# Kernel optimization log

Hardware: AMD Instinct MI355X
Metric: run time of the kernel (lower is better)

## Reference

```python
import jax, jax.numpy as jnp
import numpy as np

B, H, T, D = 4, 8, 4096, 64
NC = 64      # num_clusters
WSZ = 128    # window_size (== context_window_size)
MEM = 1      # num_mem_kv
EPS = 1e-5   # scatter_mean eps


def setup_inputs() -> dict:
    key = jax.random.key(0)
    kq, kk, kv, km, kmk, kmv = jax.random.split(key, 6)
    return {
        "q": jax.random.normal(kq, (B, H, T, D), jnp.float32),
        "k": jax.random.normal(kk, (B, H, T, D), jnp.float32),
        "v": jax.random.normal(kv, (B, H, T, D), jnp.float32),
        "means": jax.random.normal(km, (H, NC, D), jnp.float32),
        "mem_key": jax.random.normal(kmk, (H, NC, MEM, D), jnp.float32),
        "mem_value": jax.random.normal(kmv, (H, NC, MEM, D), jnp.float32),
    }


def reference(q, k, v, means, mem_key, mem_value):
    b, h, t, d = q.shape
    kv_t = k.shape[2]
    nc = means.shape[1]
    wsz = min(WSZ, t)
    kv_wsz = min(WSZ, kv_t)

    # --- kmeans routing (eval mode: no update, world_size=1) ---
    x = jnp.concatenate([q, k], axis=2)                       # (b,h,t+kv_t,d)
    norm = jnp.linalg.norm(x, axis=-1, keepdims=True)
    xn = x / jnp.maximum(norm, 1e-12)                          # F.normalize
    dists = jnp.einsum('bhld,hcd->bhlc', xn, means)            # (b,h,L,nc)
    buckets = jnp.argmax(dists, axis=-1)                       # (b,h,L)
    routed = means[jnp.arange(h)[None, :, None], buckets]      # (b,h,L,d)
    aux_loss = jnp.mean((xn - routed) ** 2)                    # mse / world_size(=1)

    dists = jax.lax.stop_gradient(dists)                       # torch no_grad
    q_dists, k_dists = dists[:, :, :t], dists[:, :, t:]

    def top_idx(dd, w):
        # dd: (b,h,L,nc) -> per-cluster top-w token indices, (b,h,nc*w)
        _, idx = jax.lax.top_k(jnp.swapaxes(dd, -1, -2), w)    # (b,h,nc,w)
        return idx.reshape(idx.shape[0], idx.shape[1], -1)

    indices = top_idx(q_dists, wsz)                            # (b,h,nc*wsz)
    kv_indices = top_idx(k_dists, kv_wsz)

    gather = lambda arr, idx: jnp.take_along_axis(arr, idx[..., None], axis=2)
    qg = gather(q, indices).reshape(b, h, nc, wsz, d)
    kg = gather(k, kv_indices).reshape(b, h, nc, kv_wsz, d)
    vg = gather(v, kv_indices).reshape(b, h, nc, kv_wsz, d)

    m_k = jnp.broadcast_to(mem_key[None], (b,) + mem_key.shape)
    m_v = jnp.broadcast_to(mem_value[None], (b,) + mem_value.shape)
    kg = jnp.concatenate([m_k, kg], axis=3)                    # (b,h,nc,MEM+kv_wsz,d)
    vg = jnp.concatenate([m_v, vg], axis=3)

    dots = jnp.einsum('bhnid,bhnjd->bhnij', qg, kg) * (d ** -0.5)
    attn = jax.nn.softmax(dots, axis=-1)
    bo = jnp.einsum('bhnij,bhnjd->bhnid', attn, vg)            # (b,h,nc,wsz,d)
    so = bo.reshape(b, h, nc * wsz, d)

    # scatter_mean back to token positions
    bi = jnp.arange(b)[:, None, None]
    hi = jnp.arange(h)[None, :, None]
    numer = jnp.zeros((b, h, t, d), q.dtype).at[bi, hi, indices].add(so)
    denom = jnp.zeros((b, h, t, d), q.dtype).at[bi, hi, indices].add(jnp.ones_like(so))
    out = numer / (denom + EPS)
    return out, aux_loss
```

## Files before the change

kernel.cpp:

```cpp
#include <hip/hip_runtime.h>
#include <math.h>

#define BB 4
#define HH 8
#define TT 4096
#define DD 64
#define NCC 64
#define WSZW 128
#define TPK 160
#define MEMN 1
#define KVW (MEMN + WSZW)
constexpr float EPSF = 1e-5f;
constexpr float SCALE = 0.125f;

typedef __attribute__((ext_vector_type(8))) short bf16x8;
typedef __attribute__((ext_vector_type(4))) float f32x4;

static __device__ __forceinline__ unsigned int pk2(float a, float b) {
    unsigned int r;
    asm("v_cvt_pk_bf16_f32 %0, %1, %2" : "=v"(r) : "v"(a), "v"(b));
    return r;
}
static __device__ __forceinline__ bf16x8 pack8(float4 a, float4 b) {
    union { unsigned int u[4]; bf16x8 v; } r;
    r.u[0] = pk2(a.x, a.y); r.u[1] = pk2(a.z, a.w);
    r.u[2] = pk2(b.x, b.y); r.u[3] = pk2(b.z, b.w);
    return r.v;
}
static __device__ __forceinline__ unsigned mono(float f) {
    unsigned b = __float_as_uint(f);
    return b ^ ((unsigned)(((int)b) >> 31) | 0x80000000u);
}
static __device__ __forceinline__ unsigned long long mono64(double d) {
    unsigned long long b = (unsigned long long)__double_as_longlong(d);
    return b ^ (((long long)b < 0) ? ~0ULL : 0x8000000000000000ULL);
}
static __device__ __forceinline__ float bf2f(unsigned short u) {
    return __uint_as_float(((unsigned)u) << 16);
}

__global__ __launch_bounds__(256, 4) void dists_kernel(
    const float* __restrict__ q, const float* __restrict__ k,
    const float* __restrict__ means,
    float* __restrict__ distsQ, float* __restrict__ distsK,
    float* __restrict__ aux_part, double* __restrict__ invn)
{
    __shared__ __align__(16) unsigned short mhS[64 * 64];
    __shared__ __align__(16) unsigned short mlS[64 * 64];
    __shared__ __align__(16) unsigned short xhS[64 * 64];
    __shared__ __align__(16) unsigned short xlS[64 * 64];
    __shared__ float mqS[64];
    __shared__ float ssnS[64];
    __shared__ float wMaxS[64 * 5];
    __shared__ int   wIdxS[64 * 5];

    const int chunks = (2 * TT) / 64;
    int bid0 = blockIdx.x;
    int bid = (bid0 & 7) * 512 + (bid0 >> 3);
    int bh = bid / chunks;
    int chunk = bid % chunks;
    int h = bh % HH;
    bool isQ = chunk < (TT / 64);
    int tbase = (isQ ? chunk : chunk - 64) * 64;
    const float* src = (isQ ? q : k) + ((size_t)bh * TT + tbase) * DD;
    float* dst = isQ ? distsQ : distsK;
    double* invdst = invn + (isQ ? 0 : (size_t)BB * HH * TT) + (size_t)bh * TT + tbase;

    int tid = threadIdx.x;
    int row = tid >> 2, part = tid & 3;

    {
        const float* mp = means + ((size_t)h * NCC + row) * DD + part * 16;
        float f[16];
        float msq = 0.f;
        #pragma unroll
        for (int i = 0; i < 4; ++i) {
            float4 va = *(const float4*)(mp + i * 4);
            f[i*4] = va.x; f[i*4+1] = va.y; f[i*4+2] = va.z; f[i*4+3] = va.w;
            msq += va.x*va.x + va.y*va.y + va.z*va.z + va.w*va.w;
        }
        msq += __shfl_xor(msq, 1);
        msq += __shfl_xor(msq, 2);
        if (part == 0) mqS[row] = msq;
        #pragma unroll
        for (int cc = 0; cc < 2; ++cc) {
            unsigned hw[4], lw[4];
            #pragma unroll
            for (int j2 = 0; j2 < 4; ++j2) {
                float a = f[cc*8 + j2*2], b = f[cc*8 + j2*2 + 1];
                unsigned p = pk2(a, b);
                float ha = __uint_as_float(p << 16);
                float hb = __uint_as_float(p & 0xFFFF0000u);
                hw[j2] = p; lw[j2] = pk2(a - ha, b - hb);
            }
            int ch = part * 2 + cc;
            int phys = ch ^ (row & 7);
            *reinterpret_cast<uint4*>(&mhS[row * 64 + phys * 8]) = (uint4){hw[0],hw[1],hw[2],hw[3]};
            *reinterpret_cast<uint4*>(&mlS[row * 64 + phys * 8]) = (uint4){lw[0],lw[1],lw[2],lw[3]};
        }
    }
    {
        const float* xp = src + (size_t)row * DD + part * 16;
        float f[16];
        double ssd = 0.0;
        #pragma unroll
        for (int i = 0; i < 4; ++i) {
            float4 va = *(const float4*)(xp + i * 4);
            f[i*4] = va.x; f[i*4+1] = va.y; f[i*4+2] = va.z; f[i*4+3] = va.w;
            ssd += (double)va.x*va.x + (double)va.y*va.y
                 + (double)va.z*va.z + (double)va.w*va.w;
        }
        ssd += __shfl_xor(ssd, 1);
        ssd += __shfl_xor(ssd, 2);
        double invd = 1.0 / fmax(sqrt(ssd), 1e-12);
        if (part == 0) {
            invdst[row] = invd;
            ssnS[row] = (float)(ssd * invd * invd);
        }
        float inv = (float)invd;
        #pragma unroll
        for (int i = 0; i < 16; ++i) f[i] *= inv;
        #pragma unroll
        for (int cc = 0; cc < 2; ++cc) {
            unsigned hw[4], lw[4];
            #pragma unroll
            for (int j2 = 0; j2 < 4; ++j2) {
                float a = f[cc*8 + j2*2], b = f[cc*8 + j2*2 + 1];
                unsigned p = pk2(a, b);
                float ha = __uint_as_float(p << 16);
                float hb = __uint_as_float(p & 0xFFFF0000u);
                hw[j2] = p; lw[j2] = pk2(a - ha, b - hb);
            }
            int ch = part * 2 + cc;
            int phys = ch ^ (row & 7);
            *reinterpret_cast<uint4*>(&xhS[row * 64 + phys * 8]) = (uint4){hw[0],hw[1],hw[2],hw[3]};
            *reinterpret_cast<uint4*>(&xlS[row * 64 + phys * 8]) = (uint4){lw[0],lw[1],lw[2],lw[3]};
        }
    }
    __syncthreads();

    int l = tid & 63, w = tid >> 6;
    int lr = l & 15, lg = l >> 4;

    bf16x8 mhF[2], mlF[2];
    #pragma unroll
    for (int ks = 0; ks < 2; ++ks) {
        int r2 = w * 16 + lr;
        int phys = (ks * 4 + lg) ^ (r2 & 7);
        mhF[ks] = *reinterpret_cast<const bf16x8*>(&mhS[r2 * 64 + phys * 8]);
        mlF[ks] = *reinterpret_cast<const bf16x8*>(&mlS[r2 * 64 + phys * 8]);
    }

    f32x4 accT[4];
    size_t rowb = (size_t)(bh * NCC) * TT;
    #pragma unroll
    for (int tt = 0; tt < 4; ++tt) {
        bf16x8 xhF[2], xlF[2];
        #pragma unroll
        for (int ks = 0; ks < 2; ++ks) {
            int r2 = tt * 16 + lr;
            int phys = (ks * 4 + lg) ^ (r2 & 7);
            xhF[ks] = *reinterpret_cast<const bf16x8*>(&xhS[r2 * 64 + phys * 8]);
            xlF[ks] = *reinterpret_cast<const bf16x8*>(&xlS[r2 * 64 + phys * 8]);
        }
        f32x4 a = (f32x4){0.f, 0.f, 0.f, 0.f};
        #pragma unroll
        for (int ks = 0; ks < 2; ++ks)
            a = __builtin_amdgcn_mfma_f32_16x16x32_bf16(mhF[ks], xhF[ks], a, 0, 0, 0);
        #pragma unroll
        for (int ks = 0; ks < 2; ++ks)
            a = __builtin_amdgcn_mfma_f32_16x16x32_bf16(mhF[ks], xlF[ks], a, 0, 0, 0);
        #pragma unroll
        for (int ks = 0; ks < 2; ++ks)
            a = __builtin_amdgcn_mfma_f32_16x16x32_bf16(mlF[ks], xhF[ks], a, 0, 0, 0);
        accT[tt] = a;
        #pragma unroll
        for (int r2 = 0; r2 < 4; ++r2) {
            int c = w * 16 + lg * 4 + r2;
            dst[rowb + (size_t)c * TT + tbase + tt * 16 + lr] = a[r2];
        }
    }

    #pragma unroll
    for (int tt = 0; tt < 4; ++tt) {
        float bv = accT[tt][0]; int bc = w * 16 + lg * 4;
        #pragma unroll
        for (int r2 = 1; r2 < 4; ++r2)
            if (accT[tt][r2] > bv) { bv = accT[tt][r2]; bc = w * 16 + lg * 4 + r2; }
        #pragma unroll
        for (int off = 16; off <= 32; off <<= 1) {
            float ov = __shfl_xor(bv, off);
            int   oc = __shfl_xor(bc, off);
            if (ov > bv || (ov == bv && oc < bc)) { bv = ov; bc = oc; }
        }
        if (lg == 0) {
            wMaxS[(tt * 16 + lr) * 5 + w] = bv;
            wIdxS[(tt * 16 + lr) * 5 + w] = bc;
        }
    }
    __syncthreads();

    if (tid < 64) {
        float bv = -1e30f; int bc = 0;
        #pragma unroll
        for (int w2 = 0; w2 < 4; ++w2) {
            float ov = wMaxS[tid * 5 + w2];
            int   oc = wIdxS[tid * 5 + w2];
            if (ov > bv || (ov == bv && oc < bc)) { bv = ov; bc = oc; }
        }
        float auxv = ssnS[tid] + mqS[bc] - 2.f * bv;
        #pragma unroll
        for (int off = 32; off; off >>= 1) auxv += __shfl_xor(auxv, off);
        if (tid == 0) aux_part[bid] = auxv;
    }
}

__global__ __launch_bounds__(256) void topk_kernel(
    const float* __restrict__ dists, int* __restrict__ idxOut)
{
    int row = blockIdx.x;
    const float* dv = dists + (size_t)row * TT;
    int t = threadIdx.x;
    int lane = t & 63, w = t >> 6;

    unsigned u[16];
    #pragma unroll
    for (int j0 = 0; j0 < 4; ++j0) {
        float4 f = *(const float4*)(dv + t * 16 + j0 * 4);
        u[j0*4+0] = mono(f.x); u[j0*4+1] = mono(f.y);
        u[j0*4+2] = mono(f.z); u[j0*4+3] = mono(f.w);
    }

    __shared__ int hist[4096];
    __shared__ int wtot[4];
    __shared__ int binSel, tgtS;
    __shared__ int nGtS, posS, eqPos;

    int target = TPK;
    unsigned prefix = 0;

    #pragma unroll
    for (int pass = 0; pass < 2; ++pass) {
        int4* hz = (int4*)&hist[t * 16];
        hz[0] = (int4){0,0,0,0}; hz[1] = (int4){0,0,0,0};
        hz[2] = (int4){0,0,0,0}; hz[3] = (int4){0,0,0,0};
        __syncthreads();
        if (pass == 0) {
            #pragma unroll
            for (int j = 0; j < 16; ++j) atomicAdd(&hist[u[j] >> 20], 1);
        } else {
            #pragma unroll
            for (int j = 0; j < 16; ++j)
                if ((u[j] >> 20) == (prefix >> 20))
                    atomicAdd(&hist[(u[j] >> 8) & 0xFFF], 1);
        }
        __syncthreads();
        int cnt[16], ls[16];
        {
            const int4* hp = (const int4*)&hist[t * 16];
            int4 c0 = hp[0], c1 = hp[1], c2 = hp[2], c3 = hp[3];
            cnt[0]=c0.x; cnt[1]=c0.y; cnt[2]=c0.z; cnt[3]=c0.w;
            cnt[4]=c1.x; cnt[5]=c1.y; cnt[6]=c1.z; cnt[7]=c1.w;
            cnt[8]=c2.x; cnt[9]=c2.y; cnt[10]=c2.z; cnt[11]=c2.w;
            cnt[12]=c3.x; cnt[13]=c3.y; cnt[14]=c3.z; cnt[15]=c3.w;
        }
        int run = 0;
        #pragma unroll
        for (int i = 15; i >= 0; --i) { run += cnt[i]; ls[i] = run; }
        int S = run;
        #pragma unroll
        for (int off = 1; off < 64; off <<= 1) {
            int o = __shfl_down(S, off);
            if (lane + off < 64) S += o;
        }
        if (lane == 0) wtot[w] = S;
        __syncthreads();
        int after = 0;
        for (int ww = w + 1; ww < 4; ++ww) after += wtot[ww];
        int St1 = S - run + after;
        #pragma unroll
        for (int i = 0; i < 16; ++i) {
            int sfxb = ls[i] + St1;
            if (sfxb >= target && sfxb - cnt[i] < target) {
                binSel = t * 16 + i; tgtS = target - (sfxb - cnt[i]);
            }
        }
        __syncthreads();
        prefix |= (pass == 0) ? ((unsigned)binSel << 20) : ((unsigned)binSel << 8);
        target = tgtS;
        __syncthreads();
    }

    hist[t] = 0;
    __syncthreads();
    #pragma unroll
    for (int j = 0; j < 16; ++j)
        if ((u[j] >> 8) == (prefix >> 8))
            atomicAdd(&hist[u[j] & 0xFF], 1);
    __syncthreads();
    {
        int cnt = hist[t];
        int S = cnt;
        #pragma unroll
        for (int off = 1; off < 64; off <<= 1) {
            int o = __shfl_down(S, off);
            if (lane + off < 64) S += o;
        }
        if (lane == 0) wtot[w] = S;
        __syncthreads();
        int after = 0;
        for (int ww = w + 1; ww < 4; ++ww) after += wtot[ww];
        int sfx = S + after;
        if (sfx >= target && sfx - cnt < target) { binSel = t; tgtS = target - (sfx - cnt); }
    }
    __syncthreads();
    unsigned pivot = prefix | (unsigned)binSel;

    if (t == 0) { nGtS = 0; posS = 0; eqPos = 0; }
    __syncthreads();
    int myg = 0;
    #pragma unroll
    for (int j = 0; j < 16; ++j) myg += (u[j] > pivot) ? 1 : 0;
    if (myg) atomicAdd(&nGtS, myg);
    __syncthreads();
    int n_gt = nGtS;
    int n_need = TPK - n_gt;
    int* out = idxOut + (size_t)row * TPK;
    #pragma unroll
    for (int j = 0; j < 16; ++j) {
        if (u[j] > pivot) {
            int p = atomicAdd(&posS, 1);
            out[p] = t * 16 + j;
        } else if (u[j] == pivot) {
            int p = atomicAdd(&eqPos, 1);
            if (p < n_need) out[n_gt + p] = t * 16 + j;
        }
    }
}

__global__ __launch_bounds__(640) void rescore_kernel(
    const float* __restrict__ q, const float* __restrict__ k,
    const float* __restrict__ means, const double* __restrict__ invn,
    const int* __restrict__ candQ, const int* __restrict__ candK,
    int* __restrict__ idxQ, int* __restrict__ idxK,
    int* __restrict__ counts)
{
    int bid = blockIdx.x;
    int rid = (bid & 7) * 512 + (bid >> 3);
    int side = rid >> 11;
    int row = rid & 2047;
    int c = row & (NCC - 1);
    int bh = row >> 6;
    int h = bh % HH;

    const int* cand = (side ? candK : candQ) + (size_t)row * TPK;
    int* outIdx     = (side ? idxK : idxQ) + (size_t)row * WSZW;
    const float* xbase = (side ? k : q) + (size_t)bh * TT * DD;
    const double* invp = invn + (side ? (size_t)BB * HH * TT : 0) + (size_t)bh * TT;

    __shared__ double   mD[DD];
    __shared__ unsigned hiS[TPK];
    __shared__ unsigned loS[TPK];
    __shared__ int      kiS[TPK];

    int tid = threadIdx.x;
    if (tid < DD) mD[tid] = (double)means[((size_t)h * NCC + c) * DD + tid];
    __syncthreads();

    int g = tid >> 2;
    int qt = tid & 3;
    int tok = cand[g];
    const float* xp = xbase + (size_t)tok * DD + qt * 16;
    double inv = invp[tok];
    double d0 = 0.0, d1 = 0.0;
    #pragma unroll
    for (int i = 0; i < 2; ++i) {
        float4 va = *(const float4*)(xp + i * 4);
        int d = qt * 16 + i * 4;
        d0 += (double)va.x * mD[d]   + (double)va.y * mD[d+1]
            + (double)va.z * mD[d+2] + (double)va.w * mD[d+3];
    }
    #pragma unroll
    for (int i = 2; i < 4; ++i) {
        float4 va = *(const float4*)(xp + i * 4);
        int d = qt * 16 + i * 4;
        d1 += (double)va.x * mD[d]   + (double)va.y * mD[d+1]
            + (double)va.z * mD[d+2] + (double)va.w * mD[d+3];
    }
    double dot = d0 + d1;
    dot += __shfl_xor(dot, 1); dot += __shfl_xor(dot, 2);
    double v = dot * inv;
    unsigned long long key = mono64(v);
    unsigned myhi = (unsigned)(key >> 32), mylo = (unsigned)key;
    if (qt == 0) { hiS[g] = myhi; loS[g] = mylo; kiS[g] = tok; }
    __syncthreads();

    int rk = 0, eq = 0;
    #pragma unroll 8
    for (int i = 0; i < TPK / 4; ++i) {
        unsigned hj = hiS[qt * (TPK / 4) + i];
        rk += (hj > myhi) ? 1 : 0;
        eq += (hj == myhi) ? 1 : 0;
    }
    rk += __shfl_xor(rk, 1); rk += __shfl_xor(rk, 2);
    eq += __shfl_xor(eq, 1); eq += __shfl_xor(eq, 2);

    if (eq > 1) {
        int rk2 = 0;
        for (int i = 0; i < TPK / 4; ++i) {
            int j = qt * (TPK / 4) + i;
            unsigned hj = hiS[j];
            if (hj > myhi) rk2++;
            else if (hj == myhi) {
                unsigned lj = loS[j];
                if (lj > mylo || (lj == mylo && kiS[j] < tok)) rk2++;
            }
        }
        rk2 += __shfl_xor(rk2, 1); rk2 += __shfl_xor(rk2, 2);
        rk = rk2;
    }

    if (qt == 0 && rk < WSZW) {
        outIdx[rk] = tok;
        if (side == 0) atomicAdd(&counts[bh * TT + tok], 1);
    }
}

__global__ __launch_bounds__(512, 8) void attn_kernel(
    const float* __restrict__ q, const float* __restrict__ k, const float* __restrict__ v,
    const float* __restrict__ mem_key, const float* __restrict__ mem_value,
    const int* __restrict__ idxQ, const int* __restrict__ idxK,
    unsigned short* __restrict__ so)
{
    int bid = blockIdx.x;
    int blk = (bid & 7) * 256 + (bid >> 3);
    int c = blk % NCC;
    int bh = blk / NCC;
    int h = bh % HH;

    __shared__ __align__(16) unsigned short KsS[130 * 64];
    __shared__ __align__(16) unsigned short VtS[64 * 168];

    int tid = threadIdx.x;
    int w = tid >> 6, l = tid & 63;
    int lr = l & 15, lg = l >> 4;

    const float* memK = mem_key   + ((size_t)h * NCC + c) * (MEMN * DD);
    const float* memV = mem_value + ((size_t)h * NCC + c) * (MEMN * DD);

    int stRow[3], stCh[3];
    const float *vsrcR[3], *ksrcR[3];
    #pragma unroll
    for (int s = 0; s < 3; ++s) {
        int idx = tid + s * 512;
        stRow[s] = idx >> 3; stCh[s] = idx & 7;
        vsrcR[s] = nullptr; ksrcR[s] = nullptr;
        if (idx < 1280 && stRow[s] < KVW) {
            if (stRow[s] == 0) { vsrcR[s] = memV; ksrcR[s] = memK; }
            else {
                int tk = idxK[(size_t)blk * WSZW + stRow[s] - 1];
                vsrcR[s] = v + ((size_t)bh * TT + tk) * DD;
                ksrcR[s] = k + ((size_t)bh * TT + tk) * DD;
            }
        }
    }

    bf16x8 qf[2];
    {
        int tq = idxQ[(size_t)blk * WSZW + w * 16 + lr];
        const float* qp = q + ((size_t)bh * TT + tq) * DD;
        #pragma unroll
        for (int ks = 0; ks < 2; ++ks) {
            float4 a = *(const float4*)(qp + ks * 32 + lg * 8);
            float4 b = *(const float4*)(qp + ks * 32 + lg * 8 + 4);
            qf[ks] = pack8(a, b);
        }
    }

    uint4 vw[3];
    #pragma unroll
    for (int s = 0; s < 3; ++s) {
        vw[s] = (uint4){0,0,0,0};
        if (vsrcR[s]) {
            float4 a = *(const float4*)(vsrcR[s] + stCh[s] * 8);
            float4 b = *(const float4*)(vsrcR[s] + stCh[s] * 8 + 4);
            vw[s].x = pk2(a.x, a.y); vw[s].y = pk2(a.z, a.w);
            vw[s].z = pk2(b.x, b.y); vw[s].w = pk2(b.z, b.w);
        }
    }
    uint4 kw[3];
    #pragma unroll
    for (int s = 0; s < 3; ++s) {
        kw[s] = (uint4){0,0,0,0};
        if (ksrcR[s]) {
            float4 a = *(const float4*)(ksrcR[s] + stCh[s] * 8);
            float4 b = *(const float4*)(ksrcR[s] + stCh[s] * 8 + 4);
            kw[s].x = pk2(a.x, a.y); kw[s].y = pk2(a.z, a.w);
            kw[s].z = pk2(b.x, b.y); kw[s].w = pk2(b.z, b.w);
        }
    }

    #pragma unroll
    for (int s = 0; s < 3; ++s)
        if (vsrcR[s])
            *reinterpret_cast<uint4*>(
                &KsS[stRow[s] * 64 + ((stCh[s] ^ (stRow[s] & 7)) * 8)]) = vw[s];
    __syncthreads();

    unsigned short vreg[3][8];
    #pragma unroll
    for (int s = 0; s < 3; ++s) {
        int idx = tid + s * 512;
        if (idx < 1280) {
            int d = idx & 63, rowblk = idx >> 6;
            #pragma unroll
            for (int i = 0; i < 8; ++i) {
                int row = rowblk * 8 + i;
                int pr = (row < KVW) ? row : 128;
                vreg[s][i] = KsS[pr * 64 + (((d >> 3) ^ (pr & 7)) * 8) + (d & 7)];
            }
        }
    }
    __syncthreads();

    #pragma unroll
    for (int s = 0; s < 3; ++s) {
        int idx = tid + s * 512;
        if (idx < 1280) {
            int d = idx & 63, rowblk = idx >> 6;
            uint4 ow;
            ow.x = (unsigned)vreg[s][0] | ((unsigned)vreg[s][1] << 16);
            ow.y = (unsigned)vreg[s][2] | ((unsigned)vreg[s][3] << 16);
            ow.z = (unsigned)vreg[s][4] | ((unsigned)vreg[s][5] << 16);
            ow.w = (unsigned)vreg[s][6] | ((unsigned)vreg[s][7] << 16);
            *reinterpret_cast<uint4*>(&VtS[d * 168 + rowblk * 8]) = ow;
        }
    }
    #pragma unroll
    for (int s = 0; s < 3; ++s)
        if (ksrcR[s])
            *reinterpret_cast<uint4*>(
                &KsS[stRow[s] * 64 + ((stCh[s] ^ (stRow[s] & 7)) * 8)]) = kw[s];
    __syncthreads();

    f32x4 acc[4];
    #pragma unroll
    for (int dt = 0; dt < 4; ++dt) acc[dt] = (f32x4){0.f, 0.f, 0.f, 0.f};
    float s_sum = 0.f;

    int src0 = lr + ((lg & 1) * 2) * 16;
    int src1 = src0 + 16;
    bool hi = (lg >> 1) != 0;

    for (int kb = 0; kb < 5; ++kb) {
        bf16x8 kf[2][2];
        #pragma unroll
        for (int kvt = 0; kvt < 2; ++kvt)
            #pragma unroll
            for (int ks = 0; ks < 2; ++ks) {
                int row = kb * 32 + kvt * 16 + lr;
                int pr = (row < KVW) ? row : 128;
                int phys = (ks * 4 + lg) ^ (pr & 7);
                kf[kvt][ks] = *reinterpret_cast<const bf16x8*>(&KsS[pr * 64 + phys * 8]);
            }
        __builtin_amdgcn_s_setprio(1);
        unsigned pk[2][2];
        #pragma unroll
        for (int kvt = 0; kvt < 2; ++kvt) {
            f32x4 sf = __builtin_amdgcn_mfma_f32_16x16x32_bf16(
                kf[kvt][0], qf[0], (f32x4){0.f,0.f,0.f,0.f}, 0, 0, 0);
            sf = __builtin_amdgcn_mfma_f32_16x16x32_bf16(kf[kvt][1], qf[1], sf, 0, 0, 0);
            float e[4];
            #pragma unroll
            for (int r = 0; r < 4; ++r) {
                int kv = kb * 32 + kvt * 16 + lg * 4 + r;
                e[r] = (kv < KVW) ? __expf(sf[r] * SCALE) : 0.f;
                s_sum += e[r];
            }
            pk[kvt][0] = pk2(e[0], e[1]);
            pk[kvt][1] = pk2(e[2], e[3]);
        }
        unsigned a00 = __shfl(pk[0][0], src0), a01 = __shfl(pk[0][1], src0);
        unsigned a10 = __shfl(pk[1][0], src0), a11 = __shfl(pk[1][1], src0);
        unsigned b00 = __shfl(pk[0][0], src1), b01 = __shfl(pk[0][1], src1);
        unsigned b10 = __shfl(pk[1][0], src1), b11 = __shfl(pk[1][1], src1);
        union { unsigned u[4]; bf16x8 v; } pu;
        pu.u[0] = hi ? a10 : a00;
        pu.u[1] = hi ? a11 : a01;
        pu.u[2] = hi ? b10 : b00;
        pu.u[3] = hi ? b11 : b01;
        #pragma unroll
        for (int dt = 0; dt < 4; ++dt) {
            bf16x8 vf = *reinterpret_cast<const bf16x8*>(
                &VtS[(dt * 16 + lr) * 168 + kb * 32 + lg * 8]);
            acc[dt] = __builtin_amdgcn_mfma_f32_16x16x32_bf16(pu.v, vf, acc[dt], 0, 0, 0);
        }
        __builtin_amdgcn_s_setprio(0);
    }

    s_sum += __shfl_xor(s_sum, 16);
    s_sum += __shfl_xor(s_sum, 32);
    float sinv[4];
    #pragma unroll
    for (int r = 0; r < 4; ++r)
        sinv[r] = 1.f / __shfl(s_sum, lg * 4 + r);

    #pragma unroll
    for (int r = 0; r < 4; ++r) {
        int row = w * 16 + lg * 4 + r;
        unsigned short* op = so + (((size_t)blk * WSZW + row) * DD);
        #pragma unroll
        for (int dt = 0; dt < 4; ++dt) {
            float ov = acc[dt][r] * sinv[r];
            op[dt * 16 + lr] = (unsigned short)(pk2(ov, ov) & 0xFFFFu);
        }
    }
}

__global__ __launch_bounds__(256) void scanfill_kernel(
    const int* __restrict__ counts, int* __restrict__ offs,
    const int* __restrict__ idxQ, int* __restrict__ csr,
    const float* __restrict__ auxp, float* __restrict__ out)
{
    __shared__ int offsL[TT];
    __shared__ int curL[TT];
    __shared__ int wsum[256];
    __shared__ float auxW[4];

    int bh = blockIdx.x;
    int t = threadIdx.x;

    float s = 0.f;
    if (bh == 0)
        for (int i = t; i < 4096; i += 256) s += auxp[i];
    #pragma unroll
    for (int off = 32; off; off >>= 1) s += __shfl_xor(s, off);
    if ((t & 63) == 0) auxW[t >> 6] = s;
    __syncthreads();
    if (bh == 0 && t == 0)
        out[(size_t)BB * HH * TT * DD] =
            (auxW[0] + auxW[1] + auxW[2] + auxW[3]) *
            (1.0f / (float)(BB * HH * 2 * TT * DD));

    const int* cb = counts + (size_t)bh * TT;
    int* ob = offs + (size_t)bh * TT;
    int loc[16]; int sum = 0;
    #pragma unroll
    for (int i = 0; i < 16; ++i) { loc[i] = sum; sum += cb[t * 16 + i]; }
    wsum[t] = sum;
    __syncthreads();
    for (int off = 1; off < 256; off <<= 1) {
        int vv = (t >= off) ? wsum[t - off] : 0;
        __syncthreads();
        wsum[t] += vv;
        __syncthreads();
    }
    int ex = (t == 0) ? 0 : wsum[t - 1];
    #pragma unroll
    for (int i = 0; i < 16; ++i) {
        int o = ex + loc[i];
        ob[t * 16 + i] = o;
        offsL[t * 16 + i] = o;
        curL[t * 16 + i] = 0;
    }
    __syncthreads();

    const int* iq = idxQ + ((size_t)bh << 13);
    int* cs = csr + ((size_t)bh << 13);
    for (int i = t; i < 8192; i += 256) {
        int tok = iq[i];
        int p = offsL[tok] + atomicAdd(&curL[tok], 1);
        cs[p] = i;
    }
}

__global__ __launch_bounds__(256) void reduce_kernel(
    const unsigned short* __restrict__ so, const int* __restrict__ counts,
    const int* __restrict__ offs, const int* __restrict__ csr,
    float* __restrict__ out)
{
    int b0 = blockIdx.x;
    int b = (b0 & 7) * 4096 + (b0 >> 3);
    int gt = b * 4 + (threadIdx.x >> 6);
    int lane = threadIdx.x & 63;
    int bh = gt >> 12;
    int n = counts[gt];
    int st = offs[gt];
    const int* cs = csr + ((size_t)bh << 13);
    const unsigned short* sob = so + (((size_t)bh << 13) * DD);
    float acc = 0.f;
    int j = 0;
    for (; j + 2 <= n; j += 2) {
        int s0 = cs[st + j], s1 = cs[st + j + 1];
        float v0 = bf2f(sob[(size_t)s0 * DD + lane]);
        float v1 = bf2f(sob[(size_t)s1 * DD + lane]);
        acc += v0 + v1;
    }
    if (j < n) acc += bf2f(sob[(size_t)cs[st + j] * DD + lane]);
    out[(size_t)gt * DD + lane] = acc / ((float)n + EPSF);
}

extern "C" void kernel_launch(void* const* d_in, const int* in_sizes, int n_in,
                              void* d_out, int out_size, void* d_ws, size_t ws_size,
                              hipStream_t stream) {
    const float* q        = (const float*)d_in[0];
    const float* k        = (const float*)d_in[1];
    const float* v        = (const float*)d_in[2];
    const float* means    = (const float*)d_in[3];
    const float* mem_key  = (const float*)d_in[4];
    const float* mem_val  = (const float*)d_in[5];
    float* out = (float*)d_out;

    const size_t nRows = (size_t)BB * HH * NCC;
    const size_t nTok  = (size_t)BB * HH * TT;
    float* wsf    = (float*)d_ws;
    float* distsQ = wsf;
    float* distsK = distsQ + (size_t)BB * HH * NCC * TT;
    unsigned short* so = (unsigned short*)wsf;
    int*   idxQ   = (int*)(distsK + (size_t)BB * HH * NCC * TT);
    int*   idxK   = idxQ + nRows * WSZW;
    int*   counts = idxK + nRows * WSZW;
    float* auxp   = (float*)(counts + nTok);
    int*   offs   = (int*)(auxp + 4096);
    int*   csr    = offs + nTok;
    int*   candQ  = csr + nTok * 2;
    int*   candK  = candQ + nRows * TPK;
    uintptr_t ip  = (uintptr_t)(candK + nRows * TPK);
    ip = (ip + 15) & ~(uintptr_t)15;
    double* invn  = (double*)ip;

    hipMemsetAsync(counts, 0, nTok * sizeof(int), stream);

    dists_kernel<<<dim3(BB * HH * (2 * TT / 64)), dim3(256), 0, stream>>>(
        q, k, means, distsQ, distsK, auxp, invn);
    topk_kernel<<<dim3((unsigned)(2 * nRows)), dim3(256), 0, stream>>>(distsQ, candQ);
    rescore_kernel<<<dim3((unsigned)(2 * nRows)), dim3(640), 0, stream>>>(
        q, k, means, invn, candQ, candK, idxQ, idxK, counts);
    scanfill_kernel<<<dim3(BB * HH), dim3(256), 0, stream>>>(
        counts, offs, idxQ, csr, auxp, out);
    attn_kernel<<<dim3((unsigned)nRows), dim3(512), 0, stream>>>(
        q, k, v, mem_key, mem_val, idxQ, idxK, so);
    reduce_kernel<<<dim3((unsigned)(nTok / 4)), dim3(256), 0, stream>>>(
        so, counts, offs, csr, out);
}
```

Before: 191.9 us.

## Store routing distances as bf16 and simplify radix top-k to 16-bit keys

The distance matrix is now written as bf16 instead of fp32, which halves the global traffic between the distance kernel and the top-k kernel. Top-k drops from a three-pass 32-bit radix select to a 12-bit plus 4-bit select over 16-bit monotone keys. The memset of the counts buffer is folded into the distance kernel. This relies on the rescore stage picking exact winners from the 160 candidates; heavy ties at bf16 precision could change which candidates survive.

```diff
diff --git a/kernel.cpp b/kernel.cpp
--- a/kernel.cpp
+++ b/kernel.cpp
@@ -27,9 +27,8 @@
     r.u[2] = pk2(b.x, b.y); r.u[3] = pk2(b.z, b.w);
     return r.v;
 }
-static __device__ __forceinline__ unsigned mono(float f) {
-    unsigned b = __float_as_uint(f);
-    return b ^ ((unsigned)(((int)b) >> 31) | 0x80000000u);
+static __device__ __forceinline__ unsigned mono16(unsigned u) {
+    return (u ^ ((u & 0x8000u) ? 0xFFFFu : 0x8000u)) & 0xFFFFu;
 }
 static __device__ __forceinline__ unsigned long long mono64(double d) {
     unsigned long long b = (unsigned long long)__double_as_longlong(d);
@@ -42,8 +41,9 @@
 __global__ __launch_bounds__(256, 4) void dists_kernel(
     const float* __restrict__ q, const float* __restrict__ k,
     const float* __restrict__ means,
-    float* __restrict__ distsQ, float* __restrict__ distsK,
-    float* __restrict__ aux_part, double* __restrict__ invn)
+    unsigned short* __restrict__ distsQ, unsigned short* __restrict__ distsK,
+    float* __restrict__ aux_part, double* __restrict__ invn,
+    int* __restrict__ counts)
 {
     __shared__ __align__(16) unsigned short mhS[64 * 64];
     __shared__ __align__(16) unsigned short mlS[64 * 64];
@@ -63,10 +63,13 @@
     bool isQ = chunk < (TT / 64);
     int tbase = (isQ ? chunk : chunk - 64) * 64;
     const float* src = (isQ ? q : k) + ((size_t)bh * TT + tbase) * DD;
-    float* dst = isQ ? distsQ : distsK;
+    unsigned short* dst = isQ ? distsQ : distsK;
     double* invdst = invn + (isQ ? 0 : (size_t)BB * HH * TT) + (size_t)bh * TT + tbase;
 
     int tid = threadIdx.x;
+
+    if (tid < 32) counts[(size_t)bid0 * 32 + tid] = 0;
+
     int row = tid >> 2, part = tid & 3;
 
     {
@@ -177,7 +180,8 @@
         #pragma unroll
         for (int r2 = 0; r2 < 4; ++r2) {
             int c = w * 16 + lg * 4 + r2;
-            dst[rowb + (size_t)c * TT + tbase + tt * 16 + lr] = a[r2];
+            dst[rowb + (size_t)c * TT + tbase + tt * 16 + lr] =
+                (unsigned short)(pk2(a[r2], a[r2]) & 0xFFFFu);
         }
     }
 
@@ -216,19 +220,23 @@
 }
 
 __global__ __launch_bounds__(256) void topk_kernel(
-    const float* __restrict__ dists, int* __restrict__ idxOut)
+    const unsigned short* __restrict__ dists, int* __restrict__ idxOut)
 {
     int row = blockIdx.x;
-    const float* dv = dists + (size_t)row * TT;
+    const unsigned short* dv = dists + (size_t)row * TT;
     int t = threadIdx.x;
     int lane = t & 63, w = t >> 6;
 
     unsigned u[16];
-    #pragma unroll
-    for (int j0 = 0; j0 < 4; ++j0) {
-        float4 f = *(const float4*)(dv + t * 16 + j0 * 4);
-        u[j0*4+0] = mono(f.x); u[j0*4+1] = mono(f.y);
-        u[j0*4+2] = mono(f.z); u[j0*4+3] = mono(f.w);
+    {
+        const uint4* p = (const uint4*)(dv + t * 16);
+        uint4 a = p[0], b = p[1];
+        unsigned ws[8] = {a.x, a.y, a.z, a.w, b.x, b.y, b.z, b.w};
+        #pragma unroll
+        for (int i = 0; i < 8; ++i) {
+            u[i*2]   = mono16(ws[i] & 0xFFFFu);
+            u[i*2+1] = mono16(ws[i] >> 16);
+        }
     }
 
     __shared__ int hist[4096];
@@ -237,23 +245,14 @@
     __shared__ int nGtS, posS, eqPos;
 
     int target = TPK;
-    unsigned prefix = 0;
-
-    #pragma unroll
-    for (int pass = 0; pass < 2; ++pass) {
+
+    {
         int4* hz = (int4*)&hist[t * 16];
         hz[0] = (int4){0,0,0,0}; hz[1] = (int4){0,0,0,0};
         hz[2] = (int4){0,0,0,0}; hz[3] = (int4){0,0,0,0};
         __syncthreads();
-        if (pass == 0) {
-            #pragma unroll
-            for (int j = 0; j < 16; ++j) atomicAdd(&hist[u[j] >> 20], 1);
-        } else {
-            #pragma unroll
-            for (int j = 0; j < 16; ++j)
-                if ((u[j] >> 20) == (prefix >> 20))
-                    atomicAdd(&hist[(u[j] >> 8) & 0xFFF], 1);
-        }
+        #pragma unroll
+        for (int j = 0; j < 16; ++j) atomicAdd(&hist[u[j] >> 4], 1);
         __syncthreads();
         int cnt[16], ls[16];
         {
@@ -286,35 +285,29 @@
             }
         }
         __syncthreads();
-        prefix |= (pass == 0) ? ((unsigned)binSel << 20) : ((unsigned)binSel << 8);
-        target = tgtS;
-        __syncthreads();
-    }
-
-    hist[t] = 0;
+    }
+    unsigned prefix12 = (unsigned)binSel;
+    target = tgtS;
+    __syncthreads();
+
+    if (t < 16) hist[t] = 0;
     __syncthreads();
     #pragma unroll
     for (int j = 0; j < 16; ++j)
-        if ((u[j] >> 8) == (prefix >> 8))
-            atomicAdd(&hist[u[j] & 0xFF], 1);
-    __syncthreads();
-    {
+        if ((u[j] >> 4) == prefix12) atomicAdd(&hist[u[j] & 0xF], 1);
+    __syncthreads();
+    if (t < 16) {
         int cnt = hist[t];
         int S = cnt;
         #pragma unroll
-        for (int off = 1; off < 64; off <<= 1) {
+        for (int off = 1; off < 16; off <<= 1) {
             int o = __shfl_down(S, off);
-            if (lane + off < 64) S += o;
-        }
-        if (lane == 0) wtot[w] = S;
-        __syncthreads();
-        int after = 0;
-        for (int ww = w + 1; ww < 4; ++ww) after += wtot[ww];
-        int sfx = S + after;
-        if (sfx >= target && sfx - cnt < target) { binSel = t; tgtS = target - (sfx - cnt); }
-    }
-    __syncthreads();
-    unsigned pivot = prefix | (unsigned)binSel;
+            if (t + off < 16) S += o;
+        }
+        if (S >= target && S - cnt < target) binSel = t;
+    }
+    __syncthreads();
+    unsigned pivot = (prefix12 << 4) | (unsigned)binSel;
 
     if (t == 0) { nGtS = 0; posS = 0; eqPos = 0; }
     __syncthreads();
@@ -713,11 +706,11 @@
 
     const size_t nRows = (size_t)BB * HH * NCC;
     const size_t nTok  = (size_t)BB * HH * TT;
-    float* wsf    = (float*)d_ws;
-    float* distsQ = wsf;
-    float* distsK = distsQ + (size_t)BB * HH * NCC * TT;
-    unsigned short* so = (unsigned short*)wsf;
-    int*   idxQ   = (int*)(distsK + (size_t)BB * HH * NCC * TT);
+    const size_t nDist = (size_t)BB * HH * NCC * TT;
+    unsigned short* distsQ = (unsigned short*)d_ws;
+    unsigned short* distsK = distsQ + nDist;
+    unsigned short* so     = distsQ;
+    int*   idxQ   = (int*)(distsK + nDist);
     int*   idxK   = idxQ + nRows * WSZW;
     int*   counts = idxK + nRows * WSZW;
     float* auxp   = (float*)(counts + nTok);
@@ -729,10 +722,8 @@
     ip = (ip + 15) & ~(uintptr_t)15;
     double* invn  = (double*)ip;
 
-    hipMemsetAsync(counts, 0, nTok * sizeof(int), stream);
-
     dists_kernel<<<dim3(BB * HH * (2 * TT / 64)), dim3(256), 0, stream>>>(
-        q, k, means, distsQ, distsK, auxp, invn);
+        q, k, means, distsQ, distsK, auxp, invn, counts);
     topk_kernel<<<dim3((unsigned)(2 * nRows)), dim3(256), 0, stream>>>(distsQ, candQ);
     rescore_kernel<<<dim3((unsigned)(2 * nRows)), dim3(640), 0, stream>>>(
         q, k, means, invn, candQ, candK, idxQ, idxK, counts);
```

Result: faster. 173.4 us (-9.6%).
